# Performance work log

Measured on AMD Instinct MI355X. Metric: run time of the kernel, lower is better.

## Reference

```python
import jax, jax.numpy as jnp
import numpy as np

VX, VY = 0.16, 0.16
PC = (0.0, -39.68, -3.0, 69.12, 39.68, 1.0)
X_OFFSET = VX / 2 + PC[0]
Y_OFFSET = VY / 2 + PC[1]
X_L = int((PC[3] - PC[0]) / VX)   # 432
Y_L = int((PC[4] - PC[1]) / VY)   # 496
C = 64
BN_EPS = 1e-3
LN_EPS = 1e-5


def setup_inputs() -> dict:
    key = jax.random.key(0)
    ks = jax.random.split(key, 16)
    B, PPB, M = 4, 10000, 32
    P = B * PPB
    # unique (x,y) pillar coords per batch, sorted by batch index (matches per-batch loop order)
    rng = np.random.default_rng(0)
    coords = []
    for i in range(B):
        lin = rng.choice(X_L * Y_L, PPB, replace=False)
        coords.append(np.stack([np.full(PPB, i), lin // Y_L, lin % Y_L], axis=1))
    coors_batch = jnp.asarray(np.concatenate(coords, axis=0), dtype=jnp.int32)
    npoints_per_pillar = jax.random.randint(ks[0], (P,), 1, M + 1, dtype=jnp.int32)
    lo = jnp.array([0.5, -39.68, -3.0, 0.0], jnp.float32)
    hi = jnp.array([69.12, 39.68, 1.0, 1.0], jnp.float32)
    pts = lo + jax.random.uniform(ks[1], (P, M, 4), dtype=jnp.float32) * (hi - lo)
    valid = (jnp.arange(M)[None, :] < npoints_per_pillar[:, None])[:, :, None]
    pillars = pts * valid  # zero-padded beyond npoints, as real voxelizers produce
    H_IMG, W_IMG = 192, 640  # half-resolution image feature map
    batch_image_map = jax.random.normal(ks[2], (B, C, H_IMG, W_IMG), dtype=jnp.float32)
    # pinhole-style 3x4 projection with forward-x as depth: u=(cx*x - fx*y)/x, v=(cy*x - fy*z)/x
    fx, fy, cx, cy = 700.0, 700.0, 640.0, 192.0
    calib = jnp.array([[cx, -fx, 0.0, 0.0], [cy, 0.0, -fy, 0.0], [1.0, 0.0, 0.0, 0.0]], jnp.float32)
    batched_calibs = jnp.tile(calib[None], (B, 1, 1)) * (1.0 + 0.01 * jax.random.normal(ks[3], (B, 3, 4)))
    conv_w = 0.1 * jax.random.normal(ks[4], (C, 9), dtype=jnp.float32)
    bn_gamma = 1.0 + 0.1 * jax.random.normal(ks[5], (C,), dtype=jnp.float32)
    bn_beta = 0.1 * jax.random.normal(ks[6], (C,), dtype=jnp.float32)
    bn_mean = 0.1 * jax.random.normal(ks[7], (C,), dtype=jnp.float32)
    bn_var = jax.random.uniform(ks[8], (C,), minval=0.5, maxval=1.5, dtype=jnp.float32)
    g_w1 = 0.1 * jax.random.normal(ks[9], (2 * C, 2 * C), dtype=jnp.float32)
    g_b1 = 0.1 * jax.random.normal(ks[10], (2 * C,), dtype=jnp.float32)
    ln_gamma = 1.0 + 0.1 * jax.random.normal(ks[11], (2 * C,), dtype=jnp.float32)
    ln_beta = 0.1 * jax.random.normal(ks[12], (2 * C,), dtype=jnp.float32)
    g_w2 = 0.1 * jax.random.normal(ks[13], (C, 2 * C), dtype=jnp.float32)
    g_b2 = 0.1 * jax.random.normal(ks[14], (C,), dtype=jnp.float32)
    return dict(pillars=pillars, coors_batch=coors_batch, npoints_per_pillar=npoints_per_pillar,
                batch_image_map=batch_image_map, batched_calibs=batched_calibs, batch_size=B,
                conv_w=conv_w, bn_gamma=bn_gamma, bn_beta=bn_beta, bn_mean=bn_mean, bn_var=bn_var,
                g_w1=g_w1, g_b1=g_b1, ln_gamma=ln_gamma, ln_beta=ln_beta, g_w2=g_w2, g_b2=g_b2)


def reference(pillars, coors_batch, npoints_per_pillar, batch_image_map, batched_calibs, batch_size,
              conv_w, bn_gamma, bn_beta, bn_mean, bn_var, g_w1, g_b1, ln_gamma, ln_beta, g_w2, g_b2):
    P, M, _ = pillars.shape
    npts = npoints_per_pillar.astype(pillars.dtype)
    mean_center = jnp.sum(pillars[:, :, :3], axis=1, keepdims=True) / npts[:, None, None]  # [P,1,3]
    offset_pt_center = pillars[:, :, :3] - mean_center
    cx = coors_batch[:, None, 1:2].astype(pillars.dtype) * VX + X_OFFSET
    cy = coors_batch[:, None, 2:3].astype(pillars.dtype) * VY + Y_OFFSET
    x_off = pillars[:, :, 0:1] - cx
    y_off = pillars[:, :, 1:2] - cy
    # channels 0,1 of the original concat are overwritten with x_off,y_off in-place
    features = jnp.concatenate([x_off, y_off, pillars[:, :, 2:], offset_pt_center, x_off, y_off], axis=-1)  # [P,M,9]
    mask = jnp.arange(M)[None, :] < npoints_per_pillar[:, None]
    features = features * mask[:, :, None]
    # Conv1d(k=1, no bias) + BatchNorm1d(eval) + ReLU (double ReLU in source collapses to one)
    h = jnp.einsum('pmi,ci->pmc', features, conv_w)
    h = (h - bn_mean) * (bn_gamma / jnp.sqrt(bn_var + BN_EPS)) + bn_beta
    h = jax.nn.relu(h)
    pooling_features = jnp.max(h, axis=1)  # [P,C]
    # vectorized image-feature gather (coors sorted by batch idx, so order matches the per-batch loop)
    bidx = coors_batch[:, 0]
    ctr = mean_center[:, 0, :]  # [P,3]
    hom = jnp.concatenate([ctr, jnp.ones((P, 1), ctr.dtype)], axis=-1)  # [P,4]
    proj = jnp.einsum('pij,pj->pi', batched_calibs[bidx], hom)
    depth = proj[:, 2]
    u = proj[:, 0] / depth
    v = proj[:, 1] / depth
    h_img, w_img = batch_image_map.shape[2], batch_image_map.shape[3]
    u = jnp.clip(u / 2, 0, w_img - 1).astype(jnp.int32)
    v = jnp.clip(v / 2, 0, h_img - 1).astype(jnp.int32)
    image_features = batch_image_map.transpose(0, 2, 3, 1)[bidx, v, u]  # [P,C]
    # gated fusion
    cat = jnp.concatenate([pooling_features, image_features], axis=1)  # [P,2C]
    g = cat @ g_w1.T + g_b1
    mu = jnp.mean(g, axis=-1, keepdims=True)
    var = jnp.var(g, axis=-1, keepdims=True)
    g = (g - mu) / jnp.sqrt(var + LN_EPS) * ln_gamma + ln_beta
    g = jax.nn.relu(g)
    gate = jax.nn.sigmoid(g @ g_w2.T + g_b2)  # [P,C]
    gate_features = pooling_features * gate + image_features * (1.0 - gate)
    # scatter to dense BEV canvas [B, x_l, y_l, C] then permute to [B, C, y_l, x_l]
    canvas = jnp.zeros((batch_size, X_L, Y_L, C), dtype=jnp.float32)
    canvas = canvas.at[bidx, coors_batch[:, 1], coors_batch[:, 2]].set(gate_features)
    return canvas.transpose(0, 3, 2, 1)
```

## Files before the change

kernel.cpp:

```cpp
#include <hip/hip_runtime.h>
#include <cfloat>
#include <cmath>

#define XL 432
#define YL 496
#define NCH 64
#define HIMG 192
#define WIMG 640
#define PTS_M 32

#define WAVES 16
#define TPB (WAVES * 64)
#define PPG 4
#define NBLOCKS 256
#define WPITCH 132

typedef const __attribute__((address_space(1))) void* gas_t;
typedef __attribute__((address_space(3))) void* las_t;

__device__ __forceinline__ void gload_lds16(const float* g, float* l) {
    __builtin_amdgcn_global_load_lds((gas_t)g, (las_t)l, 16, 0, 0);
}

#define RED5(v) { v += __shfl_xor(v, 16); v += __shfl_xor(v, 8); v += __shfl_xor(v, 4); \
                  v += __shfl_xor(v, 2);  v += __shfl_xor(v, 1); }

template<bool ATOMIC>
__global__ __launch_bounds__(TPB, 4) void pillar_fused(
    const float* __restrict__ pillars,
    const int*   __restrict__ coors,
    const int*   __restrict__ npp,
    const float* __restrict__ image,
    const float* __restrict__ calibs,
    const float* __restrict__ conv_w,
    const float* __restrict__ bng, const float* __restrict__ bnb,
    const float* __restrict__ bnm, const float* __restrict__ bnv,
    const float* __restrict__ w1, const float* __restrict__ b1,
    const float* __restrict__ lng, const float* __restrict__ lnb,
    const float* __restrict__ w2, const float* __restrict__ b2,
    float* __restrict__ out, int P, int* __restrict__ cnt)
{
    __shared__ float w1p[128 * WPITCH];
    __shared__ float w2p[64 * WPITCH];
    __shared__ float ws[WAVES][512];

    const int tid  = threadIdx.x;
    const int lane = tid & 63;
    const int wv   = tid >> 6;

    for (int i = tid; i < 128 * 32; i += TPB) {
        const int j = i >> 5, k4 = i & 31;
        ((float4*)(w1p + j * WPITCH))[k4] = ((const float4*)w1)[i];
    }
    for (int i = tid; i < 64 * 32; i += TPB) {
        const int j = i >> 5, k4 = i & 31;
        ((float4*)(w2p + j * WPITCH))[k4] = ((const float4*)w2)[i];
    }
    __syncthreads();

    float cw[9];
    #pragma unroll
    for (int i = 0; i < 9; ++i) cw[i] = conv_w[lane * 9 + i];
    const float s   = bng[lane] / sqrtf(bnv[lane] + 1e-3f);
    const float tch = bnb[lane] - bnm[lane] * s;
    const float As  = (cw[0] + cw[4] + cw[7]) * s;
    const float Bs  = (cw[1] + cw[5] + cw[8]) * s;
    const float Cs  = (cw[2] + cw[6]) * s;
    const float Ds  = cw[3] * s;
    const float w07 = (cw[0] + cw[7]) * s;
    const float w18 = (cw[1] + cw[8]) * s;
    const float w4s = cw[4] * s, w5s = cw[5] * s, w6s = cw[6] * s;

    const float b1a = b1[lane], b1b = b1[lane + 64];
    const float lga = lng[lane], lgb = lng[lane + 64];
    const float lba = lnb[lane], lbb = lnb[lane + 64];
    const float gb2 = b2[lane];

    float* wsw = ws[wv];
    const float4* wsf4 = (const float4*)wsw;
    const float4* w1rA = (const float4*)(w1p + lane * WPITCH);
    const float4* w1rB = (const float4*)(w1p + (lane + 64) * WPITCH);
    const float4* w2r  = (const float4*)(w2p + lane * WPITCH);

    const int ntasks = (P + PPG - 1) / PPG;
    int nextStatic = blockIdx.x * WAVES + wv;

    for (;;) {
        int grp;
        if (ATOMIC) {
            int g0 = 0;
            if (lane == 0) g0 = atomicAdd(cnt, 1);
            grp = __shfl(g0, 0);
        } else {
            grp = nextStatic;
            nextStatic += gridDim.x * WAVES;
        }
        if (grp >= ntasks) break;

        const int pbase = grp * PPG;
        const bool full = (pbase + PPG <= P);

        asm volatile("s_waitcnt lgkmcnt(0)" ::: "memory");
        if (full) {
            const float* src = pillars + (size_t)pbase * (PTS_M * 4);
            gload_lds16(src + lane * 4, wsw);
            gload_lds16(src + 256 + lane * 4, wsw + 256);
        } else {
            #pragma unroll
            for (int h = 0; h < 2; ++h) {
                const int idx = pbase * PTS_M + h * 64 + lane;
                float4 v = make_float4(0.f, 0.f, 0.f, 0.f);
                if (idx < P * PTS_M) v = ((const float4*)pillars)[idx];
                ((float4*)wsw)[h * 64 + lane] = v;
            }
        }

        int bbv[PPG], ixv[PPG], iyv[PPG], nv[PPG];
        #pragma unroll
        for (int pp = 0; pp < PPG; ++pp) {
            const int p = pbase + pp;
            if (p < P) {
                bbv[pp] = coors[p * 3]; ixv[pp] = coors[p * 3 + 1];
                iyv[pp] = coors[p * 3 + 2]; nv[pp] = npp[p];
            } else {
                bbv[pp] = 0; ixv[pp] = 0; iyv[pp] = 0; nv[pp] = 1;
            }
        }

        asm volatile("s_waitcnt vmcnt(0) lgkmcnt(0)" ::: "memory");

        const float4 qa = wsf4[lane];
        const float4 qb = wsf4[64 + lane];
        float ax = qa.x, ay = qa.y, az = qa.z;
        float bx = qb.x, by = qb.y, bz = qb.z;
        RED5(ax) RED5(ay) RED5(az)
        RED5(bx) RED5(by) RED5(bz)
        const float axo = __shfl_xor(ax, 32), ayo = __shfl_xor(ay, 32), azo = __shfl_xor(az, 32);
        const float bxo = __shfl_xor(bx, 32), byo = __shfl_xor(by, 32), bzo = __shfl_xor(bz, 32);
        const bool lo = lane < 32;
        float mx[PPG], my[PPG], mz[PPG];
        {
            const float f0 = 1.f / (float)nv[0], f1 = 1.f / (float)nv[1];
            const float f2 = 1.f / (float)nv[2], f3 = 1.f / (float)nv[3];
            mx[0] = (lo ? ax : axo) * f0;  mx[1] = (lo ? axo : ax) * f1;
            my[0] = (lo ? ay : ayo) * f0;  my[1] = (lo ? ayo : ay) * f1;
            mz[0] = (lo ? az : azo) * f0;  mz[1] = (lo ? azo : az) * f1;
            mx[2] = (lo ? bx : bxo) * f2;  mx[3] = (lo ? bxo : bx) * f3;
            my[2] = (lo ? by : byo) * f2;  my[3] = (lo ? byo : by) * f3;
            mz[2] = (lo ? bz : bzo) * f2;  mz[3] = (lo ? bzo : bz) * f3;
        }

        float img[PPG], Es[PPG];
        #pragma unroll
        for (int pp = 0; pp < PPG; ++pp) {
            const float* cb = calibs + bbv[pp] * 12;
            const float pr0 = cb[0]*mx[pp] + cb[1]*my[pp] + cb[2]*mz[pp] + cb[3];
            const float pr1 = cb[4]*mx[pp] + cb[5]*my[pp] + cb[6]*mz[pp] + cb[7];
            const float pr2 = cb[8]*mx[pp] + cb[9]*my[pp] + cb[10]*mz[pp] + cb[11];
            float uf = (pr0 / pr2) * 0.5f;
            float vf = (pr1 / pr2) * 0.5f;
            uf = fminf(fmaxf(uf, 0.f), (float)(WIMG - 1));
            vf = fminf(fmaxf(vf, 0.f), (float)(HIMG - 1));
            const int u = (int)uf, v = (int)vf;
            img[pp] = image[(((bbv[pp] * NCH) + lane) * HIMG + v) * WIMG + u];

            const float cxp = (float)ixv[pp] * 0.16f + 0.08f;
            const float cyp = (float)iyv[pp] * 0.16f + (-39.6f);
            Es[pp] = tch - (cxp * w07 + cyp * w18 + mx[pp] * w4s + my[pp] * w5s + mz[pp] * w6s);
        }

        float pooled[PPG];
        #pragma unroll
        for (int pp = 0; pp < PPG; ++pp) {
            const int n = nv[pp];
            float p0 = (n < PTS_M) ? tch : -FLT_MAX;
            float p1 = -FLT_MAX, p2 = -FLT_MAX, p3 = -FLT_MAX;
            #pragma unroll
            for (int m = 0; m < PTS_M; m += 4) {
                const float4 q0 = wsf4[pp * 32 + m];
                const float4 q1 = wsf4[pp * 32 + m + 1];
                const float4 q2 = wsf4[pp * 32 + m + 2];
                const float4 q3 = wsf4[pp * 32 + m + 3];
                const float h0 = Es[pp] + q0.x*As + q0.y*Bs + q0.z*Cs + q0.w*Ds;
                const float h1 = Es[pp] + q1.x*As + q1.y*Bs + q1.z*Cs + q1.w*Ds;
                const float h2 = Es[pp] + q2.x*As + q2.y*Bs + q2.z*Cs + q2.w*Ds;
                const float h3 = Es[pp] + q3.x*As + q3.y*Bs + q3.z*Cs + q3.w*Ds;
                p0 = fmaxf(p0, (m     < n) ? h0 : -FLT_MAX);
                p1 = fmaxf(p1, (m + 1 < n) ? h1 : -FLT_MAX);
                p2 = fmaxf(p2, (m + 2 < n) ? h2 : -FLT_MAX);
                p3 = fmaxf(p3, (m + 3 < n) ? h3 : -FLT_MAX);
            }
            pooled[pp] = fmaxf(fmaxf(fmaxf(p0, p1), fmaxf(p2, p3)), 0.f);
        }

        #pragma unroll
        for (int pp = 0; pp < PPG; ++pp) {
            wsw[pp * 128 + lane]      = pooled[pp];
            wsw[pp * 128 + 64 + lane] = img[pp];
        }
        asm volatile("s_waitcnt lgkmcnt(0)" ::: "memory");

        float accA[PPG], accB[PPG];
        #pragma unroll
        for (int pp = 0; pp < PPG; ++pp) { accA[pp] = b1a; accB[pp] = b1b; }
        #pragma unroll 4
        for (int k4 = 0; k4 < 32; ++k4) {
            const float4 wa = w1rA[k4];
            const float4 wb = w1rB[k4];
            #pragma unroll
            for (int pp = 0; pp < PPG; ++pp) {
                const float4 cv = wsf4[pp * 32 + k4];
                accA[pp] += cv.x*wa.x + cv.y*wa.y + cv.z*wa.z + cv.w*wa.w;
                accB[pp] += cv.x*wb.x + cv.y*wb.y + cv.z*wb.z + cv.w*wb.w;
            }
        }

        float sum[PPG], sq[PPG];
        #pragma unroll
        for (int pp = 0; pp < PPG; ++pp) {
            sum[pp] = accA[pp] + accB[pp];
            sq[pp]  = accA[pp]*accA[pp] + accB[pp]*accB[pp];
        }
        #pragma unroll
        for (int d = 32; d; d >>= 1) {
            #pragma unroll
            for (int pp = 0; pp < PPG; ++pp) {
                sum[pp] += __shfl_xor(sum[pp], d);
                sq[pp]  += __shfl_xor(sq[pp], d);
            }
        }
        #pragma unroll
        for (int pp = 0; pp < PPG; ++pp) {
            const float mu  = sum[pp] * (1.f / 128.f);
            const float var = sq[pp] * (1.f / 128.f) - mu * mu;
            const float inv = 1.f / sqrtf(var + 1e-5f);
            const float g0 = (accA[pp] - mu) * inv * lga + lba;
            const float g1 = (accB[pp] - mu) * inv * lgb + lbb;
            wsw[pp * 128 + lane]      = fmaxf(g0, 0.f);
            wsw[pp * 128 + 64 + lane] = fmaxf(g1, 0.f);
        }
        asm volatile("s_waitcnt lgkmcnt(0)" ::: "memory");

        float ac2[PPG];
        #pragma unroll
        for (int pp = 0; pp < PPG; ++pp) ac2[pp] = gb2;
        #pragma unroll 4
        for (int k4 = 0; k4 < 32; ++k4) {
            const float4 w = w2r[k4];
            #pragma unroll
            for (int pp = 0; pp < PPG; ++pp) {
                const float4 gv = wsf4[pp * 32 + k4];
                ac2[pp] += gv.x*w.x + gv.y*w.y + gv.z*w.z + gv.w*w.w;
            }
        }
        #pragma unroll
        for (int pp = 0; pp < PPG; ++pp) {
            const int p = pbase + pp;
            if (p >= P) continue;
            const float gate = 1.f / (1.f + expf(-ac2[pp]));
            const float gf = pooled[pp] * gate + img[pp] * (1.f - gate);
            out[(((bbv[pp] * NCH) + lane) * YL + iyv[pp]) * XL + ixv[pp]] = gf;
        }
    }
}

extern "C" void kernel_launch(void* const* d_in, const int* in_sizes, int n_in,
                              void* d_out, int out_size, void* d_ws, size_t ws_size,
                              hipStream_t stream)
{
    const float* pillars = (const float*)d_in[0];
    const int*   coors   = (const int*)d_in[1];
    const int*   npp     = (const int*)d_in[2];
    const float* image   = (const float*)d_in[3];
    const float* calibs  = (const float*)d_in[4];
    const float* conv_w  = (const float*)d_in[6];
    const float* bng     = (const float*)d_in[7];
    const float* bnb     = (const float*)d_in[8];
    const float* bnm     = (const float*)d_in[9];
    const float* bnv     = (const float*)d_in[10];
    const float* w1      = (const float*)d_in[11];
    const float* b1      = (const float*)d_in[12];
    const float* lng     = (const float*)d_in[13];
    const float* lnb     = (const float*)d_in[14];
    const float* w2      = (const float*)d_in[15];
    const float* b2      = (const float*)d_in[16];
    float* out = (float*)d_out;
    const int P = in_sizes[0] / (PTS_M * 4);

    hipMemsetAsync(d_out, 0, (size_t)out_size * sizeof(float), stream);
    if (ws_size >= 4) {
        hipMemsetAsync(d_ws, 0, 4, stream);
        pillar_fused<true><<<dim3(NBLOCKS), dim3(TPB), 0, stream>>>(
            pillars, coors, npp, image, calibs, conv_w, bng, bnb, bnm, bnv,
            w1, b1, lng, lnb, w2, b2, out, P, (int*)d_ws);
    } else {
        pillar_fused<false><<<dim3(NBLOCKS), dim3(TPB), 0, stream>>>(
            pillars, coors, npp, image, calibs, conv_w, bng, bnb, bnm, bnv,
            w1, b1, lng, lnb, w2, b2, out, P, nullptr);
    }
}
```

Baseline: 224.3 us.

## Replace zero-memset plus scatter with compact features and a gather canvas build

The fused kernel now writes gate features compactly to a workspace buffer, along with a pillar index map. A second kernel builds each canvas row by gathering from those features and writes coalesced float4 rows, which replaces the full-output memset and the strided scattered writes. Pillar data and intermediate activations are now broadcast with readlane instead of being staged through LDS, and the atomic work counter is replaced by a static grid-stride schedule. This adds an extra kernel, an index-map memset and a gather read of the features, and readlane broadcasts add scalar-path overhead.

Result: slower. 725.9 us (+223.7%).

```diff
diff --git a/kernel.cpp b/kernel.cpp
--- a/kernel.cpp
+++ b/kernel.cpp
@@ -15,18 +15,22 @@
 #define NBLOCKS 256
 #define WPITCH 132
 
-typedef const __attribute__((address_space(1))) void* gas_t;
-typedef __attribute__((address_space(3))) void* las_t;
-
-__device__ __forceinline__ void gload_lds16(const float* g, float* l) {
-    __builtin_amdgcn_global_load_lds((gas_t)g, (las_t)l, 16, 0, 0);
+__device__ __forceinline__ float rl(float v, int l) {
+    return __uint_as_float(__builtin_amdgcn_readlane(__float_as_uint(v), l));
 }
 
 #define RED5(v) { v += __shfl_xor(v, 16); v += __shfl_xor(v, 8); v += __shfl_xor(v, 4); \
                   v += __shfl_xor(v, 2);  v += __shfl_xor(v, 1); }
 
-template<bool ATOMIC>
-__global__ __launch_bounds__(TPB, 4) void pillar_fused(
+__global__ void zerofill(float4* __restrict__ o, int n4) {
+    int i = blockIdx.x * blockDim.x + threadIdx.x;
+    const int st = gridDim.x * blockDim.x;
+    const float4 z = make_float4(0.f, 0.f, 0.f, 0.f);
+    for (; i < n4; i += st) o[i] = z;
+}
+
+template<bool DIRECT>
+__global__ __launch_bounds__(TPB, 4) void pillar_compute(
     const float* __restrict__ pillars,
     const int*   __restrict__ coors,
     const int*   __restrict__ npp,
@@ -38,11 +42,11 @@
     const float* __restrict__ w1, const float* __restrict__ b1,
     const float* __restrict__ lng, const float* __restrict__ lnb,
     const float* __restrict__ w2, const float* __restrict__ b2,
-    float* __restrict__ out, int P, int* __restrict__ cnt)
+    float* __restrict__ feat, int* __restrict__ idxmap,
+    float* __restrict__ out, int P)
 {
     __shared__ float w1p[128 * WPITCH];
     __shared__ float w2p[64 * WPITCH];
-    __shared__ float ws[WAVES][512];
 
     const int tid  = threadIdx.x;
     const int lane = tid & 63;
@@ -76,43 +80,24 @@
     const float lba = lnb[lane], lbb = lnb[lane + 64];
     const float gb2 = b2[lane];
 
-    float* wsw = ws[wv];
-    const float4* wsf4 = (const float4*)wsw;
     const float4* w1rA = (const float4*)(w1p + lane * WPITCH);
     const float4* w1rB = (const float4*)(w1p + (lane + 64) * WPITCH);
     const float4* w2r  = (const float4*)(w2p + lane * WPITCH);
 
     const int ntasks = (P + PPG - 1) / PPG;
-    int nextStatic = blockIdx.x * WAVES + wv;
-
-    for (;;) {
-        int grp;
-        if (ATOMIC) {
-            int g0 = 0;
-            if (lane == 0) g0 = atomicAdd(cnt, 1);
-            grp = __shfl(g0, 0);
+
+    for (int grp = blockIdx.x * WAVES + wv; grp < ntasks; grp += NBLOCKS * WAVES) {
+        const int pbase = grp * PPG;
+
+        const float4* pb4 = (const float4*)pillars + (size_t)pbase * PTS_M;
+        float4 qa, qb;
+        if (pbase + PPG <= P) {
+            qa = pb4[lane];
+            qb = pb4[lane + 64];
         } else {
-            grp = nextStatic;
-            nextStatic += gridDim.x * WAVES;
-        }
-        if (grp >= ntasks) break;
-
-        const int pbase = grp * PPG;
-        const bool full = (pbase + PPG <= P);
-
-        asm volatile("s_waitcnt lgkmcnt(0)" ::: "memory");
-        if (full) {
-            const float* src = pillars + (size_t)pbase * (PTS_M * 4);
-            gload_lds16(src + lane * 4, wsw);
-            gload_lds16(src + 256 + lane * 4, wsw + 256);
-        } else {
-            #pragma unroll
-            for (int h = 0; h < 2; ++h) {
-                const int idx = pbase * PTS_M + h * 64 + lane;
-                float4 v = make_float4(0.f, 0.f, 0.f, 0.f);
-                if (idx < P * PTS_M) v = ((const float4*)pillars)[idx];
-                ((float4*)wsw)[h * 64 + lane] = v;
-            }
+            const int lim = (P - pbase) * PTS_M;
+            qa = (lane      < lim) ? pb4[lane]      : make_float4(0.f,0.f,0.f,0.f);
+            qb = (lane + 64 < lim) ? pb4[lane + 64] : make_float4(0.f,0.f,0.f,0.f);
         }
 
         int bbv[PPG], ixv[PPG], iyv[PPG], nv[PPG];
@@ -122,15 +107,9 @@
             if (p < P) {
                 bbv[pp] = coors[p * 3]; ixv[pp] = coors[p * 3 + 1];
                 iyv[pp] = coors[p * 3 + 2]; nv[pp] = npp[p];
-            } else {
-                bbv[pp] = 0; ixv[pp] = 0; iyv[pp] = 0; nv[pp] = 1;
-            }
-        }
-
-        asm volatile("s_waitcnt vmcnt(0) lgkmcnt(0)" ::: "memory");
-
-        const float4 qa = wsf4[lane];
-        const float4 qb = wsf4[64 + lane];
+            } else { bbv[pp] = 0; ixv[pp] = 0; iyv[pp] = 0; nv[pp] = 1; }
+        }
+
         float ax = qa.x, ay = qa.y, az = qa.z;
         float bx = qb.x, by = qb.y, bz = qb.z;
         RED5(ax) RED5(ay) RED5(az)
@@ -162,7 +141,7 @@
             uf = fminf(fmaxf(uf, 0.f), (float)(WIMG - 1));
             vf = fminf(fmaxf(vf, 0.f), (float)(HIMG - 1));
             const int u = (int)uf, v = (int)vf;
-            img[pp] = image[(((bbv[pp] * NCH) + lane) * HIMG + v) * WIMG + u];
+            img[pp] = image[(((size_t)(bbv[pp] * NCH + lane)) * HIMG + v) * WIMG + u];
 
             const float cxp = (float)ixv[pp] * 0.16f + 0.08f;
             const float cyp = (float)iyv[pp] * 0.16f + (-39.6f);
@@ -172,19 +151,17 @@
         float pooled[PPG];
         #pragma unroll
         for (int pp = 0; pp < PPG; ++pp) {
+            const float4& qr = (pp < 2) ? qa : qb;
+            const int lb = (pp & 1) * 32;
             const int n = nv[pp];
             float p0 = (n < PTS_M) ? tch : -FLT_MAX;
             float p1 = -FLT_MAX, p2 = -FLT_MAX, p3 = -FLT_MAX;
             #pragma unroll
             for (int m = 0; m < PTS_M; m += 4) {
-                const float4 q0 = wsf4[pp * 32 + m];
-                const float4 q1 = wsf4[pp * 32 + m + 1];
-                const float4 q2 = wsf4[pp * 32 + m + 2];
-                const float4 q3 = wsf4[pp * 32 + m + 3];
-                const float h0 = Es[pp] + q0.x*As + q0.y*Bs + q0.z*Cs + q0.w*Ds;
-                const float h1 = Es[pp] + q1.x*As + q1.y*Bs + q1.z*Cs + q1.w*Ds;
-                const float h2 = Es[pp] + q2.x*As + q2.y*Bs + q2.z*Cs + q2.w*Ds;
-                const float h3 = Es[pp] + q3.x*As + q3.y*Bs + q3.z*Cs + q3.w*Ds;
+                const float h0 = Es[pp] + rl(qr.x,lb+m  )*As + rl(qr.y,lb+m  )*Bs + rl(qr.z,lb+m  )*Cs + rl(qr.w,lb+m  )*Ds;
+                const float h1 = Es[pp] + rl(qr.x,lb+m+1)*As + rl(qr.y,lb+m+1)*Bs + rl(qr.z,lb+m+1)*Cs + rl(qr.w,lb+m+1)*Ds;
+                const float h2 = Es[pp] + rl(qr.x,lb+m+2)*As + rl(qr.y,lb+m+2)*Bs + rl(qr.z,lb+m+2)*Cs + rl(qr.w,lb+m+2)*Ds;
+                const float h3 = Es[pp] + rl(qr.x,lb+m+3)*As + rl(qr.y,lb+m+3)*Bs + rl(qr.z,lb+m+3)*Cs + rl(qr.w,lb+m+3)*Ds;
                 p0 = fmaxf(p0, (m     < n) ? h0 : -FLT_MAX);
                 p1 = fmaxf(p1, (m + 1 < n) ? h1 : -FLT_MAX);
                 p2 = fmaxf(p2, (m + 2 < n) ? h2 : -FLT_MAX);
@@ -193,74 +170,121 @@
             pooled[pp] = fmaxf(fmaxf(fmaxf(p0, p1), fmaxf(p2, p3)), 0.f);
         }
 
-        #pragma unroll
-        for (int pp = 0; pp < PPG; ++pp) {
-            wsw[pp * 128 + lane]      = pooled[pp];
-            wsw[pp * 128 + 64 + lane] = img[pp];
-        }
-        asm volatile("s_waitcnt lgkmcnt(0)" ::: "memory");
-
         float accA[PPG], accB[PPG];
         #pragma unroll
         for (int pp = 0; pp < PPG; ++pp) { accA[pp] = b1a; accB[pp] = b1b; }
-        #pragma unroll 4
-        for (int k4 = 0; k4 < 32; ++k4) {
+        #pragma unroll
+        for (int k4 = 0; k4 < 16; ++k4) {
             const float4 wa = w1rA[k4];
             const float4 wb = w1rB[k4];
             #pragma unroll
             for (int pp = 0; pp < PPG; ++pp) {
-                const float4 cv = wsf4[pp * 32 + k4];
-                accA[pp] += cv.x*wa.x + cv.y*wa.y + cv.z*wa.z + cv.w*wa.w;
-                accB[pp] += cv.x*wb.x + cv.y*wb.y + cv.z*wb.z + cv.w*wb.w;
-            }
-        }
-
-        float sum[PPG], sq[PPG];
-        #pragma unroll
-        for (int pp = 0; pp < PPG; ++pp) {
-            sum[pp] = accA[pp] + accB[pp];
-            sq[pp]  = accA[pp]*accA[pp] + accB[pp]*accB[pp];
-        }
-        #pragma unroll
-        for (int d = 32; d; d >>= 1) {
-            #pragma unroll
-            for (int pp = 0; pp < PPG; ++pp) {
-                sum[pp] += __shfl_xor(sum[pp], d);
-                sq[pp]  += __shfl_xor(sq[pp], d);
-            }
-        }
-        #pragma unroll
-        for (int pp = 0; pp < PPG; ++pp) {
-            const float mu  = sum[pp] * (1.f / 128.f);
-            const float var = sq[pp] * (1.f / 128.f) - mu * mu;
-            const float inv = 1.f / sqrtf(var + 1e-5f);
-            const float g0 = (accA[pp] - mu) * inv * lga + lba;
-            const float g1 = (accB[pp] - mu) * inv * lgb + lbb;
-            wsw[pp * 128 + lane]      = fmaxf(g0, 0.f);
-            wsw[pp * 128 + 64 + lane] = fmaxf(g1, 0.f);
-        }
-        asm volatile("s_waitcnt lgkmcnt(0)" ::: "memory");
+                const float s0 = rl(pooled[pp], 4*k4+0), s1 = rl(pooled[pp], 4*k4+1);
+                const float s2 = rl(pooled[pp], 4*k4+2), s3 = rl(pooled[pp], 4*k4+3);
+                accA[pp] += s0*wa.x + s1*wa.y + s2*wa.z + s3*wa.w;
+                accB[pp] += s0*wb.x + s1*wb.y + s2*wb.z + s3*wb.w;
+            }
+        }
+        #pragma unroll
+        for (int k4 = 0; k4 < 16; ++k4) {
+            const float4 wa = w1rA[16 + k4];
+            const float4 wb = w1rB[16 + k4];
+            #pragma unroll
+            for (int pp = 0; pp < PPG; ++pp) {
+                const float s0 = rl(img[pp], 4*k4+0), s1 = rl(img[pp], 4*k4+1);
+                const float s2 = rl(img[pp], 4*k4+2), s3 = rl(img[pp], 4*k4+3);
+                accA[pp] += s0*wa.x + s1*wa.y + s2*wa.z + s3*wa.w;
+                accB[pp] += s0*wb.x + s1*wb.y + s2*wb.z + s3*wb.w;
+            }
+        }
+
+        float gA[PPG], gB[PPG];
+        {
+            float sum[PPG], sq[PPG];
+            #pragma unroll
+            for (int pp = 0; pp < PPG; ++pp) {
+                sum[pp] = accA[pp] + accB[pp];
+                sq[pp]  = accA[pp]*accA[pp] + accB[pp]*accB[pp];
+            }
+            #pragma unroll
+            for (int d = 32; d; d >>= 1) {
+                #pragma unroll
+                for (int pp = 0; pp < PPG; ++pp) {
+                    sum[pp] += __shfl_xor(sum[pp], d);
+                    sq[pp]  += __shfl_xor(sq[pp], d);
+                }
+            }
+            #pragma unroll
+            for (int pp = 0; pp < PPG; ++pp) {
+                const float mu  = sum[pp] * (1.f / 128.f);
+                const float var = sq[pp] * (1.f / 128.f) - mu * mu;
+                const float inv = 1.f / sqrtf(var + 1e-5f);
+                gA[pp] = fmaxf((accA[pp] - mu) * inv * lga + lba, 0.f);
+                gB[pp] = fmaxf((accB[pp] - mu) * inv * lgb + lbb, 0.f);
+            }
+        }
 
         float ac2[PPG];
         #pragma unroll
         for (int pp = 0; pp < PPG; ++pp) ac2[pp] = gb2;
-        #pragma unroll 4
-        for (int k4 = 0; k4 < 32; ++k4) {
+        #pragma unroll
+        for (int k4 = 0; k4 < 16; ++k4) {
             const float4 w = w2r[k4];
             #pragma unroll
             for (int pp = 0; pp < PPG; ++pp) {
-                const float4 gv = wsf4[pp * 32 + k4];
-                ac2[pp] += gv.x*w.x + gv.y*w.y + gv.z*w.z + gv.w*w.w;
-            }
-        }
+                ac2[pp] += rl(gA[pp],4*k4+0)*w.x + rl(gA[pp],4*k4+1)*w.y
+                         + rl(gA[pp],4*k4+2)*w.z + rl(gA[pp],4*k4+3)*w.w;
+            }
+        }
+        #pragma unroll
+        for (int k4 = 0; k4 < 16; ++k4) {
+            const float4 w = w2r[16 + k4];
+            #pragma unroll
+            for (int pp = 0; pp < PPG; ++pp) {
+                ac2[pp] += rl(gB[pp],4*k4+0)*w.x + rl(gB[pp],4*k4+1)*w.y
+                         + rl(gB[pp],4*k4+2)*w.z + rl(gB[pp],4*k4+3)*w.w;
+            }
+        }
+
         #pragma unroll
         for (int pp = 0; pp < PPG; ++pp) {
             const int p = pbase + pp;
             if (p >= P) continue;
             const float gate = 1.f / (1.f + expf(-ac2[pp]));
             const float gf = pooled[pp] * gate + img[pp] * (1.f - gate);
-            out[(((bbv[pp] * NCH) + lane) * YL + iyv[pp]) * XL + ixv[pp]] = gf;
-        }
+            if (DIRECT) {
+                out[(((bbv[pp] * NCH) + lane) * YL + iyv[pp]) * XL + ixv[pp]] = gf;
+            } else {
+                feat[(size_t)p * NCH + lane] = gf;
+                if (lane == 0)
+                    idxmap[(bbv[pp] * YL + iyv[pp]) * XL + ixv[pp]] = p + 1;
+            }
+        }
+    }
+}
+
+__global__ __launch_bounds__(256) void canvas_build(
+    const float* __restrict__ feat, const int* __restrict__ idxmap,
+    float4* __restrict__ out)
+{
+    __shared__ int idxrow[XL];
+    const int by = blockIdx.x;
+    const int b = by / YL, y = by % YL;
+    const int* irow = idxmap + (size_t)by * XL;
+    for (int i = threadIdx.x; i < XL; i += 256) idxrow[i] = irow[i];
+    __syncthreads();
+
+    const int NF4 = XL / 4;
+    for (int t = threadIdx.x; t < NCH * NF4; t += 256) {
+        const int c = t / NF4, x4 = t - c * NF4;
+        const int i0 = idxrow[x4*4+0], i1 = idxrow[x4*4+1];
+        const int i2 = idxrow[x4*4+2], i3 = idxrow[x4*4+3];
+        float4 o = make_float4(0.f, 0.f, 0.f, 0.f);
+        if (i0) o.x = feat[(size_t)(i0-1) * NCH + c];
+        if (i1) o.y = feat[(size_t)(i1-1) * NCH + c];
+        if (i2) o.z = feat[(size_t)(i2-1) * NCH + c];
+        if (i3) o.w = feat[(size_t)(i3-1) * NCH + c];
+        out[((size_t)(b * NCH + c) * YL + y) * NF4 + x4] = o;
     }
 }
 
@@ -286,16 +310,23 @@
     const float* b2      = (const float*)d_in[16];
     float* out = (float*)d_out;
     const int P = in_sizes[0] / (PTS_M * 4);
-
-    hipMemsetAsync(d_out, 0, (size_t)out_size * sizeof(float), stream);
-    if (ws_size >= 4) {
-        hipMemsetAsync(d_ws, 0, 4, stream);
-        pillar_fused<true><<<dim3(NBLOCKS), dim3(TPB), 0, stream>>>(
+    const int B = in_sizes[3] / (NCH * HIMG * WIMG);
+
+    const size_t featBytes = (size_t)P * NCH * sizeof(float);
+    const size_t idxBytes  = (size_t)B * YL * XL * sizeof(int);
+
+    if (ws_size >= featBytes + idxBytes) {
+        float* feat = (float*)d_ws;
+        int* idxmap = (int*)((char*)d_ws + featBytes);
+        hipMemsetAsync(idxmap, 0, idxBytes, stream);
+        pillar_compute<false><<<dim3(NBLOCKS), dim3(TPB), 0, stream>>>(
             pillars, coors, npp, image, calibs, conv_w, bng, bnb, bnm, bnv,
-            w1, b1, lng, lnb, w2, b2, out, P, (int*)d_ws);
+            w1, b1, lng, lnb, w2, b2, feat, idxmap, nullptr, P);
+        canvas_build<<<dim3(B * YL), dim3(256), 0, stream>>>(feat, idxmap, (float4*)d_out);
     } else {
-        pillar_fused<false><<<dim3(NBLOCKS), dim3(TPB), 0, stream>>>(
+        zerofill<<<dim3(2048), dim3(256), 0, stream>>>((float4*)d_out, out_size / 4);
+        pillar_compute<true><<<dim3(NBLOCKS), dim3(TPB), 0, stream>>>(
             pillars, coors, npp, image, calibs, conv_w, bng, bnb, bnm, bnv,
-            w1, b1, lng, lnb, w2, b2, out, P, nullptr);
-    }
-}
+            w1, b1, lng, lnb, w2, b2, nullptr, nullptr, out, P);
+    }
+}
```

## Transpose image to channels-last and build BEV canvas via gather pass

Applied to the files above, without the earlier changes.

Adds a tiled transpose that turns the image map into channels-last layout, so each pillar's 64-channel image lookup becomes one contiguous read instead of 64 strided ones. The fused kernel now writes per-pillar features to a compact buffer plus an index map. A separate canvas_build kernel then streams the whole output in coalesced float4 rows, filling zeros and gathering features. This replaces the output memset and the scattered strided stores, at the cost of a full-image transpose pass and extra workspace; fallback paths are chosen by workspace size.

Result: faster. 212.0 us (-5.5%).

```diff
diff --git a/kernel.cpp b/kernel.cpp
--- a/kernel.cpp
+++ b/kernel.cpp
@@ -7,6 +7,7 @@
 #define NCH 64
 #define HIMG 192
 #define WIMG 640
+#define HW (HIMG * WIMG)
 #define PTS_M 32
 
 #define WAVES 16
@@ -25,20 +26,49 @@
 #define RED5(v) { v += __shfl_xor(v, 16); v += __shfl_xor(v, 8); v += __shfl_xor(v, 4); \
                   v += __shfl_xor(v, 2);  v += __shfl_xor(v, 1); }
 
-template<bool ATOMIC>
-__global__ __launch_bounds__(TPB, 4) void pillar_fused(
-    const float* __restrict__ pillars,
-    const int*   __restrict__ coors,
-    const int*   __restrict__ npp,
-    const float* __restrict__ image,
-    const float* __restrict__ calibs,
-    const float* __restrict__ conv_w,
+__global__ void zerofill(float4* __restrict__ o, int n4) {
+    int i = blockIdx.x * blockDim.x + threadIdx.x;
+    const int st = gridDim.x * blockDim.x;
+    const float4 z = make_float4(0.f, 0.f, 0.f, 0.f);
+    for (; i < n4; i += st) o[i] = z;
+}
+
+__global__ __launch_bounds__(256) void transpose_cl(
+    const float* __restrict__ img, float* __restrict__ imgT)
+{
+    __shared__ float t[64 * 257];
+    const int b    = blockIdx.x / (HW / 256);
+    const int tile = blockIdx.x % (HW / 256);
+    const int hw0  = tile * 256;
+    const int tid  = threadIdx.x;
+
+    const float* base = img + (size_t)b * NCH * HW + hw0;
+    #pragma unroll 4
+    for (int c = 0; c < 64; ++c)
+        t[c * 257 + tid] = base[(size_t)c * HW + tid];
+    __syncthreads();
+
+    float* ob = imgT + ((size_t)b * HW + hw0) * NCH;
+    const int c = tid & 63, r = tid >> 6;
+    #pragma unroll 4
+    for (int it = 0; it < 64; ++it) {
+        const int hw = it * 4 + r;
+        ob[hw * 64 + c] = t[c * 257 + hw];
+    }
+}
+
+template<int MODE>
+__global__ __launch_bounds__(TPB, 4) void pillar_compute(
+    const float* __restrict__ pillars, const int* __restrict__ coors,
+    const int* __restrict__ npp, const float* __restrict__ image,
+    const float* __restrict__ calibs, const float* __restrict__ conv_w,
     const float* __restrict__ bng, const float* __restrict__ bnb,
     const float* __restrict__ bnm, const float* __restrict__ bnv,
     const float* __restrict__ w1, const float* __restrict__ b1,
     const float* __restrict__ lng, const float* __restrict__ lnb,
     const float* __restrict__ w2, const float* __restrict__ b2,
-    float* __restrict__ out, int P, int* __restrict__ cnt)
+    float* __restrict__ feat, int* __restrict__ idxmap,
+    float* __restrict__ out, int P)
 {
     __shared__ float w1p[128 * WPITCH];
     __shared__ float w2p[64 * WPITCH];
@@ -83,20 +113,8 @@
     const float4* w2r  = (const float4*)(w2p + lane * WPITCH);
 
     const int ntasks = (P + PPG - 1) / PPG;
-    int nextStatic = blockIdx.x * WAVES + wv;
-
-    for (;;) {
-        int grp;
-        if (ATOMIC) {
-            int g0 = 0;
-            if (lane == 0) g0 = atomicAdd(cnt, 1);
-            grp = __shfl(g0, 0);
-        } else {
-            grp = nextStatic;
-            nextStatic += gridDim.x * WAVES;
-        }
-        if (grp >= ntasks) break;
-
+
+    for (int grp = blockIdx.x * WAVES + wv; grp < ntasks; grp += NBLOCKS * WAVES) {
         const int pbase = grp * PPG;
         const bool full = (pbase + PPG <= P);
 
@@ -122,9 +140,7 @@
             if (p < P) {
                 bbv[pp] = coors[p * 3]; ixv[pp] = coors[p * 3 + 1];
                 iyv[pp] = coors[p * 3 + 2]; nv[pp] = npp[p];
-            } else {
-                bbv[pp] = 0; ixv[pp] = 0; iyv[pp] = 0; nv[pp] = 1;
-            }
+            } else { bbv[pp] = 0; ixv[pp] = 0; iyv[pp] = 0; nv[pp] = 1; }
         }
 
         asm volatile("s_waitcnt vmcnt(0) lgkmcnt(0)" ::: "memory");
@@ -162,8 +178,11 @@
             uf = fminf(fmaxf(uf, 0.f), (float)(WIMG - 1));
             vf = fminf(fmaxf(vf, 0.f), (float)(HIMG - 1));
             const int u = (int)uf, v = (int)vf;
-            img[pp] = image[(((bbv[pp] * NCH) + lane) * HIMG + v) * WIMG + u];
-
+            if (MODE == 2) {
+                img[pp] = image[((size_t)bbv[pp] * HW + (size_t)v * WIMG + u) * NCH + lane];
+            } else {
+                img[pp] = image[(((size_t)(bbv[pp] * NCH + lane)) * HIMG + v) * WIMG + u];
+            }
             const float cxp = (float)ixv[pp] * 0.16f + 0.08f;
             const float cyp = (float)iyv[pp] * 0.16f + (-39.6f);
             Es[pp] = tch - (cxp * w07 + cyp * w18 + mx[pp] * w4s + my[pp] * w5s + mz[pp] * w6s);
@@ -259,8 +278,39 @@
             if (p >= P) continue;
             const float gate = 1.f / (1.f + expf(-ac2[pp]));
             const float gf = pooled[pp] * gate + img[pp] * (1.f - gate);
-            out[(((bbv[pp] * NCH) + lane) * YL + iyv[pp]) * XL + ixv[pp]] = gf;
-        }
+            if (MODE == 0) {
+                out[(((bbv[pp] * NCH) + lane) * YL + iyv[pp]) * XL + ixv[pp]] = gf;
+            } else {
+                feat[(size_t)p * NCH + lane] = gf;
+                if (lane == 0)
+                    idxmap[(bbv[pp] * YL + iyv[pp]) * XL + ixv[pp]] = p + 1;
+            }
+        }
+    }
+}
+
+__global__ __launch_bounds__(256) void canvas_build(
+    const float* __restrict__ feat, const int* __restrict__ idxmap,
+    float4* __restrict__ out)
+{
+    __shared__ int idxrow[XL];
+    const int by = blockIdx.x;
+    const int b = by / YL, y = by % YL;
+    const int* irow = idxmap + (size_t)by * XL;
+    for (int i = threadIdx.x; i < XL; i += 256) idxrow[i] = irow[i];
+    __syncthreads();
+
+    const int NF4 = XL / 4;
+    for (int t = threadIdx.x; t < NCH * NF4; t += 256) {
+        const int c = t / NF4, x4 = t - c * NF4;
+        const int i0 = idxrow[x4*4+0], i1 = idxrow[x4*4+1];
+        const int i2 = idxrow[x4*4+2], i3 = idxrow[x4*4+3];
+        float4 o = make_float4(0.f, 0.f, 0.f, 0.f);
+        if (i0) o.x = feat[(size_t)(i0-1) * NCH + c];
+        if (i1) o.y = feat[(size_t)(i1-1) * NCH + c];
+        if (i2) o.z = feat[(size_t)(i2-1) * NCH + c];
+        if (i3) o.w = feat[(size_t)(i3-1) * NCH + c];
+        out[((size_t)(b * NCH + c) * YL + y) * NF4 + x4] = o;
     }
 }
 
@@ -286,16 +336,34 @@
     const float* b2      = (const float*)d_in[16];
     float* out = (float*)d_out;
     const int P = in_sizes[0] / (PTS_M * 4);
-
-    hipMemsetAsync(d_out, 0, (size_t)out_size * sizeof(float), stream);
-    if (ws_size >= 4) {
-        hipMemsetAsync(d_ws, 0, 4, stream);
-        pillar_fused<true><<<dim3(NBLOCKS), dim3(TPB), 0, stream>>>(
+    const int B = in_sizes[3] / (NCH * HW);
+
+    const size_t featBytes = (size_t)P * NCH * sizeof(float);
+    const size_t idxBytes  = (size_t)B * YL * XL * sizeof(int);
+    const size_t imgTBytes = (size_t)B * HW * NCH * sizeof(float);
+
+    if (ws_size >= featBytes + idxBytes + imgTBytes) {
+        float* feat   = (float*)d_ws;
+        int*   idxmap = (int*)((char*)d_ws + featBytes);
+        float* imgT   = (float*)((char*)d_ws + featBytes + idxBytes);
+        hipMemsetAsync(idxmap, 0, idxBytes, stream);
+        transpose_cl<<<dim3(B * (HW / 256)), dim3(256), 0, stream>>>(image, imgT);
+        pillar_compute<2><<<dim3(NBLOCKS), dim3(TPB), 0, stream>>>(
+            pillars, coors, npp, imgT, calibs, conv_w, bng, bnb, bnm, bnv,
+            w1, b1, lng, lnb, w2, b2, feat, idxmap, nullptr, P);
+        canvas_build<<<dim3(B * YL), dim3(256), 0, stream>>>(feat, idxmap, (float4*)d_out);
+    } else if (ws_size >= featBytes + idxBytes) {
+        float* feat   = (float*)d_ws;
+        int*   idxmap = (int*)((char*)d_ws + featBytes);
+        hipMemsetAsync(idxmap, 0, idxBytes, stream);
+        pillar_compute<1><<<dim3(NBLOCKS), dim3(TPB), 0, stream>>>(
             pillars, coors, npp, image, calibs, conv_w, bng, bnb, bnm, bnv,
-            w1, b1, lng, lnb, w2, b2, out, P, (int*)d_ws);
+            w1, b1, lng, lnb, w2, b2, feat, idxmap, nullptr, P);
+        canvas_build<<<dim3(B * YL), dim3(256), 0, stream>>>(feat, idxmap, (float4*)d_out);
     } else {
-        pillar_fused<false><<<dim3(NBLOCKS), dim3(TPB), 0, stream>>>(
+        zerofill<<<dim3(2048), dim3(256), 0, stream>>>((float4*)d_out, out_size / 4);
+        pillar_compute<0><<<dim3(NBLOCKS), dim3(TPB), 0, stream>>>(
             pillars, coors, npp, image, calibs, conv_w, bng, bnb, bnm, bnv,
-            w1, b1, lng, lnb, w2, b2, out, P, nullptr);
-    }
-}
+            w1, b1, lng, lnb, w2, b2, nullptr, nullptr, out, P);
+    }
+}
```
